# Optimization experiments

Measured on AMD Instinct MI355X. Metric: run time of the kernel, lower is better.

## Reference

```python
import jax, jax.numpy as jnp
import numpy as np

DIM = 1536
NH = 12
HD = DIM // NH          # 128
C = HD // 2             # 64 rotary pairs
F, H, W = 6, 20, 20
L = F * H * W           # 2400
B = 1
MAX_POS = 1024
EPS = 1e-6


def _rope_freqs():
    """[MAX_POS, C, 2, 2] rotation matrices, split [22,21,21] across f/h/w axes."""
    c0 = C - 2 * (C // 3)           # 22
    c1 = C // 3                      # 21
    pos = np.arange(MAX_POS, dtype=np.float32)
    parts = []
    for m in (c0, c1, c1):
        inv = 1.0 / (10000.0 ** (np.arange(m, dtype=np.float32) / m))
        parts.append(pos[:, None] * inv[None, :])
    ang = np.concatenate(parts, axis=1)          # [MAX_POS, C]
    cos, sin = np.cos(ang), np.sin(ang)
    # R[..., j, k]: rows [cos, -sin], [sin, cos]
    R = np.stack([np.stack([cos, -sin], -1), np.stack([sin, cos], -1)], -2)
    return jnp.asarray(R, dtype=jnp.float32)


def setup_inputs() -> dict:
    key = jax.random.key(0)
    ks = jax.random.split(key, 12)
    s = 1.0 / np.sqrt(DIM)
    lin = lambda k: (jax.random.normal(k, (DIM, DIM), jnp.float32) * s)
    return {
        "x": jax.random.normal(ks[0], (B, L, DIM), jnp.float32),
        "Wq": lin(ks[1]), "bq": jax.random.normal(ks[2], (DIM,), jnp.float32) * 0.01,
        "Wk": lin(ks[3]), "bk": jax.random.normal(ks[4], (DIM,), jnp.float32) * 0.01,
        "Wv": lin(ks[5]), "bv": jax.random.normal(ks[6], (DIM,), jnp.float32) * 0.01,
        "Wo": lin(ks[7]), "bo": jax.random.normal(ks[8], (DIM,), jnp.float32) * 0.01,
        "gq": jnp.ones((DIM,), jnp.float32),
        "gk": jnp.ones((DIM,), jnp.float32),
        "seq_lens": jnp.full((B,), L, dtype=jnp.int32),
        "grid_sizes": jnp.asarray([[F, H, W]], dtype=jnp.int32),
        "freqs": _rope_freqs(),
    }


def _rms_norm(x, g, eps=EPS):
    # WanRMSNorm: x * rsqrt(mean(x^2, -1) + eps) * weight
    return x * jax.lax.rsqrt(jnp.mean(jnp.square(x), axis=-1, keepdims=True) + eps) * g


def _rope_apply(xh, grid_sizes, freqs):
    """xh: [B, L, n, d]; freqs: [MAX_POS, c, 2, 2]. All samples share one grid."""
    b, l, n, d = xh.shape
    c = d // 2
    c0 = c - 2 * (c // 3)
    c1 = c // 3
    f, h, w = (int(v) for v in np.asarray(grid_sizes[0]))
    # build per-position 3D rotation matrices: [f*h*w, c, 2, 2]
    fa = jnp.broadcast_to(freqs[:f, :c0][:, None, None], (f, h, w, c0, 2, 2))
    fb = jnp.broadcast_to(freqs[:h, c0:c0 + c1][None, :, None], (f, h, w, c1, 2, 2))
    fc = jnp.broadcast_to(freqs[:w, c0 + c1:c][None, None, :], (f, h, w, c1, 2, 2))
    R = jnp.concatenate([fa, fb, fc], axis=3).reshape(f * h * w, c, 2, 2)
    xp = xh.reshape(b, l, n, c, 2)
    out = jnp.einsum('lcjk,blnck->blncj', R, xp)
    return out.reshape(b, l, n, d)


def reference(x, Wq, bq, Wk, bk, Wv, bv, Wo, bo, gq, gk, seq_lens, grid_sizes, freqs):
    b, l = x.shape[:2]
    q = _rms_norm(x @ Wq.T + bq, gq).reshape(b, l, NH, HD)
    k = _rms_norm(x @ Wk.T + bk, gk).reshape(b, l, NH, HD)
    v = (x @ Wv.T + bv).reshape(b, l, NH, HD)
    q = _rope_apply(q, grid_sizes, freqs)
    k = _rope_apply(k, grid_sizes, freqs)
    # full attention with key-length mask (window_size=(-1,-1))
    scores = jnp.einsum('bqnd,bknd->bnqk', q, k) / np.sqrt(HD)
    kmask = jnp.arange(l)[None, :] < seq_lens[:, None]          # [B, L]
    scores = jnp.where(kmask[:, None, None, :], scores, -1e9)
    attn = jax.nn.softmax(scores, axis=-1)
    out = jnp.einsum('bnqk,bknd->bqnd', attn, v).reshape(b, l, DIM)
    return out @ Wo.T + bo
```

## Files before the change

kernel.cpp:

```cpp
#include <hip/hip_runtime.h>
#include <hip/hip_bf16.h>
#include <stdint.h>


#define DIM  1536
#define NH   12
#define HD   128
#define LSEQ 2400
#define LPAD 2432
#define KT   64
#define NT   (LPAD / KT)

typedef __attribute__((ext_vector_type(8))) short short8;
typedef __attribute__((ext_vector_type(4))) float f32x4;
typedef unsigned short ushort_t;
typedef unsigned int   uint32;

__device__ __forceinline__ ushort_t f2bf(float f) {
  union { float f; unsigned u; } v; v.f = f;
  unsigned r = (v.u + 0x7fffu + ((v.u >> 16) & 1u)) >> 16;
  return (ushort_t)r;
}
__device__ __forceinline__ float bf2f(ushort_t h) {
  union { unsigned u; float f; } v; v.u = ((unsigned)h) << 16;
  return v.f;
}
__device__ __forceinline__ void async16(void* lds, const void* g) {
  __builtin_amdgcn_global_load_lds(
      (const __attribute__((address_space(1))) uint32*)g,
      (__attribute__((address_space(3))) uint32*)lds, 16, 0, 0);
}

__global__ void cvtx(const float* __restrict__ s, ushort_t* __restrict__ d)
{
  const int i = blockIdx.x * 256 + threadIdx.x;
  uint4 u = {0, 0, 0, 0};
  if (i * 8 < LSEQ * DIM) {
    float4 f0 = *(const float4*)(s + i * 8);
    float4 f1 = *(const float4*)(s + i * 8 + 4);
    u.x = (uint32)f2bf(f0.x) | ((uint32)f2bf(f0.y) << 16);
    u.y = (uint32)f2bf(f0.z) | ((uint32)f2bf(f0.w) << 16);
    u.z = (uint32)f2bf(f1.x) | ((uint32)f2bf(f1.y) << 16);
    u.w = (uint32)f2bf(f1.z) | ((uint32)f2bf(f1.w) << 16);
  }
  *(uint4*)(d + i * 8) = u;
}

__global__ void cvtw(const float* __restrict__ s0, const float* __restrict__ s1,
                     const float* __restrict__ s2, const float* __restrict__ s3,
                     ushort_t* __restrict__ d0, ushort_t* __restrict__ d1,
                     ushort_t* __restrict__ d2, ushort_t* __restrict__ d3)
{
  const int z = blockIdx.y;
  const float* s = (z == 0) ? s0 : ((z == 1) ? s1 : ((z == 2) ? s2 : s3));
  ushort_t* d    = (z == 0) ? d0 : ((z == 1) ? d1 : ((z == 2) ? d2 : d3));
  const int i = blockIdx.x * 256 + threadIdx.x;
  float4 f0 = *(const float4*)(s + i * 8);
  float4 f1 = *(const float4*)(s + i * 8 + 4);
  uint4 u;
  u.x = (uint32)f2bf(f0.x) | ((uint32)f2bf(f0.y) << 16);
  u.y = (uint32)f2bf(f0.z) | ((uint32)f2bf(f0.w) << 16);
  u.z = (uint32)f2bf(f1.x) | ((uint32)f2bf(f1.y) << 16);
  u.w = (uint32)f2bf(f1.z) | ((uint32)f2bf(f1.w) << 16);
  *(uint4*)(d + i * 8) = u;
}

template<int OUT_F32>
__global__ __launch_bounds__(256) void gemm_bt(
    const ushort_t* __restrict__ Ap,
    const ushort_t* __restrict__ B0, const ushort_t* __restrict__ B1, const ushort_t* __restrict__ B2,
    const float* __restrict__ b0, const float* __restrict__ b1, const float* __restrict__ b2,
    void* __restrict__ D0, void* __restrict__ D1, void* __restrict__ D2,
    int Mout)
{
  const int z = blockIdx.y;
  const ushort_t* Bw  = (z == 0) ? B0 : ((z == 1) ? B1 : B2);
  const float* bias   = (z == 0) ? b0 : ((z == 1) ? b1 : b2);
  void* D             = (z == 0) ? D0 : ((z == 1) ? D1 : D2);

  const int bm = blockIdx.x / 12, bn = blockIdx.x % 12;
  const int tid = threadIdx.x;
  const int w = tid >> 6, lam = tid & 63;
  const int wr = w >> 1, wc = w & 1;
  const int lane15 = lam & 15, quad = lam >> 4;

  __shared__ __align__(16) char lds[32768];
  char* sA = lds;
  char* sB = lds + 16384;

  f32x4 acc[4][4];
#pragma unroll
  for (int i = 0; i < 4; ++i)
#pragma unroll
    for (int j = 0; j < 4; ++j) acc[i][j] = {};

  const int sm = (w * 32) + (lam >> 3);
  const int sc = (lam & 7);

  for (int k0 = 0; k0 < DIM; k0 += 64) {
    __syncthreads();
#pragma unroll
    for (int i = 0; i < 4; ++i) {
      const int li = w * 4096 + i * 1024;
      const int m = sm + i * 8;
      const int c = sc ^ (m & 7);
      async16(sA + li, Ap + (size_t)(bm * 128 + m) * DIM + k0 + c * 8);
      async16(sB + li, Bw + (size_t)(bn * 128 + m) * DIM + k0 + c * 8);
    }
    __syncthreads();
#pragma unroll
    for (int kc = 0; kc < 2; ++kc) {
      const int chunk = kc * 4 + quad;
      short8 af[4], bfr[4];
#pragma unroll
      for (int i = 0; i < 4; ++i) {
        const int m = wr * 64 + i * 16 + lane15;
        af[i] = *(const short8*)(sA + m * 128 + ((chunk ^ (m & 7)) * 16));
      }
#pragma unroll
      for (int j = 0; j < 4; ++j) {
        const int n = wc * 64 + j * 16 + lane15;
        bfr[j] = *(const short8*)(sB + n * 128 + ((chunk ^ (n & 7)) * 16));
      }
#pragma unroll
      for (int i = 0; i < 4; ++i)
#pragma unroll
        for (int j = 0; j < 4; ++j)
          acc[i][j] = __builtin_amdgcn_mfma_f32_16x16x32_bf16(af[i], bfr[j], acc[i][j], 0, 0, 0);
    }
  }

#pragma unroll
  for (int j = 0; j < 4; ++j) {
    const int n = bn * 128 + wc * 64 + j * 16 + lane15;
    const float bv = bias[n];
#pragma unroll
    for (int i = 0; i < 4; ++i) {
      const int mb = bm * 128 + wr * 64 + i * 16 + quad * 4;
#pragma unroll
      for (int r = 0; r < 4; ++r) {
        const int m = mb + r;
        const float val = acc[i][j][r] + bv;
        if (OUT_F32) {
          if (m < Mout) ((float*)D)[(size_t)m * DIM + n] = val;
        } else {
          ((ushort_t*)D)[(size_t)m * DIM + n] = f2bf(val);
        }
      }
    }
  }
}

__global__ __launch_bounds__(256) void norm_rope(
    const ushort_t* __restrict__ qpre, const ushort_t* __restrict__ kpre,
    const float* __restrict__ gq, const float* __restrict__ gk,
    const float* __restrict__ freqs,
    const int* __restrict__ seq_lens, const int* __restrict__ grid_sizes,
    ushort_t* __restrict__ qh, ushort_t* __restrict__ kh)
{
  const int row = blockIdx.x;
  const int which = blockIdx.y;
  const ushort_t* src = which ? kpre : qpre;
  const float* g = which ? gk : gq;
  ushort_t* dst = which ? kh : qh;
  const int tid = threadIdx.x;

  float s = 0.f;
  if (tid < 192) {
    uint4 u = *(const uint4*)(src + (size_t)row * DIM + tid * 8);
    const uint32 uu[4] = {u.x, u.y, u.z, u.w};
#pragma unroll
    for (int i = 0; i < 4; ++i) {
      float a = bf2f((ushort_t)(uu[i] & 0xffff));
      float b = bf2f((ushort_t)(uu[i] >> 16));
      s += a * a + b * b;
    }
  }
#pragma unroll
  for (int off = 32; off; off >>= 1) s += __shfl_down(s, off, 64);
  __shared__ float wsum[4];
  __shared__ float srstd;
  if ((tid & 63) == 0) wsum[tid >> 6] = s;
  __syncthreads();
  if (tid == 0)
    srstd = rsqrtf((wsum[0] + wsum[1] + wsum[2] + wsum[3]) / (float)DIM + 1e-6f);
  __syncthreads();
  const float rstd = srstd;

  const int seq = seq_lens[0];
  const int h_ = grid_sizes[1], w_ = grid_sizes[2];
  const int hw = h_ * w_;
  const int fidx = row / hw;
  const int rem = row - fidx * hw;
  const int hidx = rem / w_;
  const int widx = rem - hidx * w_;
  const bool live = row < seq;

#pragma unroll
  for (int pp = 0; pp < 3; ++pp) {
    const int p = tid + pp * 256;
    const int c = p & 63, head = p >> 6;
    const int e_in = head * HD + 2 * c;
    uint32 xin = *(const uint32*)(src + (size_t)row * DIM + e_in);
    float x0 = bf2f((ushort_t)(xin & 0xffff));
    float x1 = bf2f((ushort_t)(xin >> 16));
    float2 gg = *(const float2*)(g + e_in);
    float y0 = x0 * rstd * gg.x, y1 = x1 * rstd * gg.y;
    const int pos = (c < 22) ? fidx : ((c < 43) ? hidx : widx);
    float4 R = *(const float4*)(freqs + ((size_t)pos * 64 + c) * 4);
    float o0 = R.x * y0 + R.y * y1;
    float o1 = R.z * y0 + R.w * y1;
    uint32 op = live ? ((uint32)f2bf(o0) | ((uint32)f2bf(o1) << 16)) : 0u;
    *(uint32*)(dst + ((size_t)head * LPAD + row) * HD + 2 * c) = op;
  }
}

__global__ void vpanel(const ushort_t* __restrict__ v, ushort_t* __restrict__ vp)
{
  const int head = blockIdx.z;
  const int d0 = blockIdx.y * 32;
  const int l0 = blockIdx.x * 32;
  __shared__ ushort_t t[32][33];
  const int tx = threadIdx.x, ty = threadIdx.y;
  t[ty][tx] = v[(size_t)(l0 + ty) * DIM + head * HD + d0 + tx];
  __syncthreads();
  const int tt = l0 >> 6;
  const int kk = (l0 & 63) + tx;
  vp[(((size_t)head * NT + tt) * HD + d0 + ty) * KT + kk] = t[tx][ty];
}

__global__ __launch_bounds__(256, 2) void attn4(
    const ushort_t* __restrict__ qh, const ushort_t* __restrict__ kh,
    const ushort_t* __restrict__ vp, const int* __restrict__ seq_lens,
    ushort_t* __restrict__ attno)
{
  const int head = blockIdx.y;
  const int q0 = blockIdx.x * 64;
  const int tid = threadIdx.x;
  const int w = tid >> 6, lam = tid & 63;
  const int lane15 = lam & 15, quad = lam >> 4;
  const int seq = seq_lens[0];

  __shared__ __align__(16) char kbuf[2][16384];
  __shared__ __align__(16) char vbuf[2][16384];
  __shared__ __align__(16) ushort_t pbuf[4][16][72];

  const ushort_t* qbase = qh + ((size_t)head * LPAD + q0 + w * 16) * HD;
  short8 qf[4];
#pragma unroll
  for (int kc = 0; kc < 4; ++kc)
    qf[kc] = *(const short8*)(qbase + lane15 * HD + kc * 32 + quad * 8);

  f32x4 o[8];
#pragma unroll
  for (int dt = 0; dt < 8; ++dt) o[dt] = {};
  float lacc[4] = {0.f, 0.f, 0.f, 0.f};

  const float scale = 0.08838834764831845f;

  const ushort_t* khh = kh + (size_t)head * LPAD * HD;
  const ushort_t* vph = vp + (size_t)head * NT * HD * KT;

  const int krow0 = w * 16 + (lam >> 4);
  const int kslot = lam & 15;
  const int vrow0 = w * 32 + (lam >> 3);
  const int vslot = lam & 7;

#define STAGE(t, b)                                                      \
  {                                                                      \
    const ushort_t* kg = khh + (size_t)(t) * (KT * HD);                  \
    const ushort_t* vg = vph + (size_t)(t) * (HD * KT);                  \
    _Pragma("unroll")                                                    \
    for (int i = 0; i < 4; ++i) {                                        \
      const int li = w * 4096 + i * 1024;                                \
      const int kr = krow0 + i * 4;                                      \
      const int kc_ = kslot ^ (kr & 15);                                 \
      async16(kbuf[b] + li, kg + kr * HD + kc_ * 8);                     \
      const int vr = vrow0 + i * 8;                                      \
      const int vc = vslot ^ (vr & 7);                                   \
      async16(vbuf[b] + li, vg + vr * KT + vc * 8);                      \
    }                                                                    \
  }

  STAGE(0, 0)
  __syncthreads();

  for (int t = 0; t < NT; ++t) {
    const int b = t & 1;
    if (t + 1 < NT) STAGE(t + 1, b ^ 1)

    f32x4 S[4];
#pragma unroll
    for (int n0 = 0; n0 < 4; ++n0) S[n0] = {};
#pragma unroll
    for (int n0 = 0; n0 < 4; ++n0)
#pragma unroll
      for (int kc = 0; kc < 4; ++kc) {
        short8 kf = *(const short8*)(kbuf[b] + (n0 * 16 + lane15) * 256 +
                                     (((kc * 4 + quad) ^ lane15) * 16));
        S[n0] = __builtin_amdgcn_mfma_f32_16x16x32_bf16(qf[kc], kf, S[n0], 0, 0, 0);
      }

#pragma unroll
    for (int n0 = 0; n0 < 4; ++n0) {
      const bool valid = (t * KT + n0 * 16 + lane15) < seq;
#pragma unroll
      for (int r = 0; r < 4; ++r) {
        float e = valid ? __expf(S[n0][r] * scale - 12.0f) : 0.f;
        lacc[r] += e;
        pbuf[w][quad * 4 + r][n0 * 16 + lane15] = f2bf(e);
      }
    }
    asm volatile("s_waitcnt lgkmcnt(0)" ::: "memory");

#pragma unroll
    for (int kc2 = 0; kc2 < 2; ++kc2) {
      short8 pf = *(const short8*)(&pbuf[w][lane15][kc2 * 32 + quad * 8]);
#pragma unroll
      for (int dt = 0; dt < 8; ++dt) {
        short8 vf = *(const short8*)(vbuf[b] + (dt * 16 + lane15) * 128 +
                                     (((kc2 * 4 + quad) ^ (lane15 & 7)) * 16));
        o[dt] = __builtin_amdgcn_mfma_f32_16x16x32_bf16(pf, vf, o[dt], 0, 0, 0);
      }
    }
    __syncthreads();
  }
#undef STAGE

  float linv[4];
#pragma unroll
  for (int r = 0; r < 4; ++r) {
    float l = lacc[r];
#pragma unroll
    for (int off = 1; off < 16; off <<= 1) l += __shfl_xor(l, off, 16);
    linv[r] = 1.0f / l;
  }
#pragma unroll
  for (int dt = 0; dt < 8; ++dt)
#pragma unroll
    for (int r = 0; r < 4; ++r) {
      const int m = q0 + w * 16 + quad * 4 + r;
      attno[(size_t)m * DIM + head * HD + dt * 16 + lane15] = f2bf(o[dt][r] * linv[r]);
    }
}

extern "C" void kernel_launch(void* const* d_in, const int* in_sizes, int n_in,
                              void* d_out, int out_size, void* d_ws, size_t ws_size,
                              hipStream_t stream)
{
  const float* x  = (const float*)d_in[0];
  const float* Wq = (const float*)d_in[1];
  const float* bq = (const float*)d_in[2];
  const float* Wk = (const float*)d_in[3];
  const float* bk = (const float*)d_in[4];
  const float* Wv = (const float*)d_in[5];
  const float* bv = (const float*)d_in[6];
  const float* Wo = (const float*)d_in[7];
  const float* bo = (const float*)d_in[8];
  const float* gq = (const float*)d_in[9];
  const float* gk = (const float*)d_in[10];
  const int* seq_lens   = (const int*)d_in[11];
  const int* grid_sizes = (const int*)d_in[12];
  const float* freqs    = (const float*)d_in[13];
  float* out = (float*)d_out;

  const size_t BUF = (size_t)LPAD * DIM * 2;
  const size_t WB  = (size_t)DIM * DIM * 2;
  char* ws = (char*)d_ws;
  dim3 blk(256);

  ushort_t* xbf  = (ushort_t*)(ws);
  ushort_t* wqb  = (ushort_t*)(ws + BUF);
  ushort_t* wkb  = (ushort_t*)(ws + BUF + WB);
  ushort_t* wvb  = (ushort_t*)(ws + BUF + 2 * WB);
  ushort_t* wob  = (ushort_t*)(ws + BUF + 3 * WB);
  ushort_t* qpre = (ushort_t*)(ws + BUF + 4 * WB);
  ushort_t* kpre = (ushort_t*)(ws + 2 * BUF + 4 * WB);
  ushort_t* qh   = (ushort_t*)(ws + 3 * BUF + 4 * WB);
  ushort_t* kh   = (ushort_t*)(ws + 4 * BUF + 4 * WB);
  ushort_t* vbf  = (ushort_t*)(ws + 5 * BUF + 4 * WB);
  ushort_t* vp    = kpre;
  ushort_t* attno = xbf;

  cvtx<<<dim3(LPAD * DIM / 2048), blk, 0, stream>>>(x, xbf);
  cvtw<<<dim3(DIM * DIM / 2048, 4), blk, 0, stream>>>(
      Wq, Wk, Wv, Wo, wqb, wkb, wvb, wob);

  gemm_bt<0><<<dim3(228, 3), blk, 0, stream>>>(
      xbf, wqb, wkb, wvb, bq, bk, bv, qpre, kpre, vbf, 0);
  norm_rope<<<dim3(LPAD, 2), blk, 0, stream>>>(
      qpre, kpre, gq, gk, freqs, seq_lens, grid_sizes, qh, kh);
  vpanel<<<dim3(LPAD / 32, HD / 32, NH), dim3(32, 32), 0, stream>>>(vbf, vp);
  attn4<<<dim3(LPAD / 64, NH), blk, 0, stream>>>(qh, kh, vp, seq_lens, attno);
  gemm_bt<1><<<dim3(228, 1), blk, 0, stream>>>(
      attno, wob, wob, wob, bo, bo, bo, out, out, out, LSEQ);
}
```

Baseline: 303.3 us.

## Split attention over two key halves with merge kernel; fuse conversion and prep kernels

Attention now splits the key sequence into two halves along a new grid dimension, doubling the block count from 456 to 912 so the GPU's compute units stay busier. Each half writes fp16 partial outputs plus row sums, and a new merge kernel combines them into bf16. The key tile shrinks to 32 and the V panel layout changes to match. The x and weight conversions are fused into one launch, and norm/rope is fused with the V transpose, cutting launches. This adds extra global traffic for the fp16 partials and the merge pass, plus some fp16 precision loss.

```diff
diff --git a/kernel.cpp b/kernel.cpp
--- a/kernel.cpp
+++ b/kernel.cpp
@@ -8,10 +8,13 @@
 #define HD   128
 #define LSEQ 2400
 #define LPAD 2432
-#define KT   64
-#define NT   (LPAD / KT)
+#define KT2  32
+#define NT2  (LPAD / KT2)
+#define NTH  38
+#define KVH  (LPAD / 2)
 
 typedef __attribute__((ext_vector_type(8))) short short8;
+typedef __attribute__((ext_vector_type(8))) _Float16 half8;
 typedef __attribute__((ext_vector_type(4))) float f32x4;
 typedef unsigned short ushort_t;
 typedef unsigned int   uint32;
@@ -30,39 +33,42 @@
       (const __attribute__((address_space(1))) uint32*)g,
       (__attribute__((address_space(3))) uint32*)lds, 16, 0, 0);
 }
-
-__global__ void cvtx(const float* __restrict__ s, ushort_t* __restrict__ d)
-{
+__device__ __forceinline__ uint4 pack8(const float* f) {
+  uint4 u;
+  u.x = (uint32)f2bf(f[0]) | ((uint32)f2bf(f[1]) << 16);
+  u.y = (uint32)f2bf(f[2]) | ((uint32)f2bf(f[3]) << 16);
+  u.z = (uint32)f2bf(f[4]) | ((uint32)f2bf(f[5]) << 16);
+  u.w = (uint32)f2bf(f[6]) | ((uint32)f2bf(f[7]) << 16);
+  return u;
+}
+
+__global__ void cvt_all(const float* __restrict__ x,
+                        const float* __restrict__ W0, const float* __restrict__ W1,
+                        const float* __restrict__ W2, const float* __restrict__ W3,
+                        ushort_t* __restrict__ xd,
+                        ushort_t* __restrict__ d0, ushort_t* __restrict__ d1,
+                        ushort_t* __restrict__ d2, ushort_t* __restrict__ d3)
+{
+  const int z = blockIdx.y;
   const int i = blockIdx.x * 256 + threadIdx.x;
-  uint4 u = {0, 0, 0, 0};
-  if (i * 8 < LSEQ * DIM) {
-    float4 f0 = *(const float4*)(s + i * 8);
-    float4 f1 = *(const float4*)(s + i * 8 + 4);
-    u.x = (uint32)f2bf(f0.x) | ((uint32)f2bf(f0.y) << 16);
-    u.y = (uint32)f2bf(f0.z) | ((uint32)f2bf(f0.w) << 16);
-    u.z = (uint32)f2bf(f1.x) | ((uint32)f2bf(f1.y) << 16);
-    u.w = (uint32)f2bf(f1.z) | ((uint32)f2bf(f1.w) << 16);
-  }
-  *(uint4*)(d + i * 8) = u;
-}
-
-__global__ void cvtw(const float* __restrict__ s0, const float* __restrict__ s1,
-                     const float* __restrict__ s2, const float* __restrict__ s3,
-                     ushort_t* __restrict__ d0, ushort_t* __restrict__ d1,
-                     ushort_t* __restrict__ d2, ushort_t* __restrict__ d3)
-{
-  const int z = blockIdx.y;
-  const float* s = (z == 0) ? s0 : ((z == 1) ? s1 : ((z == 2) ? s2 : s3));
-  ushort_t* d    = (z == 0) ? d0 : ((z == 1) ? d1 : ((z == 2) ? d2 : d3));
-  const int i = blockIdx.x * 256 + threadIdx.x;
-  float4 f0 = *(const float4*)(s + i * 8);
-  float4 f1 = *(const float4*)(s + i * 8 + 4);
-  uint4 u;
-  u.x = (uint32)f2bf(f0.x) | ((uint32)f2bf(f0.y) << 16);
-  u.y = (uint32)f2bf(f0.z) | ((uint32)f2bf(f0.w) << 16);
-  u.z = (uint32)f2bf(f1.x) | ((uint32)f2bf(f1.y) << 16);
-  u.w = (uint32)f2bf(f1.z) | ((uint32)f2bf(f1.w) << 16);
-  *(uint4*)(d + i * 8) = u;
+  if (z == 0) {
+    uint4 u = {0, 0, 0, 0};
+    if (i * 8 < LSEQ * DIM) {
+      float f[8];
+      *(float4*)f = *(const float4*)(x + i * 8);
+      *(float4*)(f + 4) = *(const float4*)(x + i * 8 + 4);
+      u = pack8(f);
+    }
+    *(uint4*)(xd + i * 8) = u;
+    return;
+  }
+  if (blockIdx.x >= DIM * DIM / 2048) return;
+  const float* s = (z == 1) ? W0 : ((z == 2) ? W1 : ((z == 3) ? W2 : W3));
+  ushort_t* d    = (z == 1) ? d0 : ((z == 2) ? d1 : ((z == 3) ? d2 : d3));
+  float f[8];
+  *(float4*)f = *(const float4*)(s + i * 8);
+  *(float4*)(f + 4) = *(const float4*)(s + i * 8 + 4);
+  *(uint4*)(d + i * 8) = pack8(f);
 }
 
 template<int OUT_F32>
@@ -151,19 +157,46 @@
   }
 }
 
-__global__ __launch_bounds__(256) void norm_rope(
+__global__ __launch_bounds__(256) void nr_vp(
     const ushort_t* __restrict__ qpre, const ushort_t* __restrict__ kpre,
+    const ushort_t* __restrict__ vbf,
     const float* __restrict__ gq, const float* __restrict__ gk,
     const float* __restrict__ freqs,
     const int* __restrict__ seq_lens, const int* __restrict__ grid_sizes,
-    ushort_t* __restrict__ qh, ushort_t* __restrict__ kh)
-{
-  const int row = blockIdx.x;
-  const int which = blockIdx.y;
+    ushort_t* __restrict__ qh, ushort_t* __restrict__ kh,
+    ushort_t* __restrict__ vp)
+{
+  const int bx = blockIdx.x;
+  const int tid = threadIdx.x;
+  __shared__ float wsum[4];
+  __shared__ float srstd;
+  __shared__ ushort_t tbuf[32][33];
+
+  if (bx >= 2 * LPAD) {
+    const int vb = bx - 2 * LPAD;
+    const int head = vb / (NT2 * 4);
+    const int rem = vb - head * (NT2 * 4);
+    const int t2 = rem >> 2;
+    const int d0 = (rem & 3) * 32;
+    const int l0 = t2 * 32;
+    const int tx = tid & 31, ty = tid >> 5;
+#pragma unroll
+    for (int rr = 0; rr < 4; ++rr)
+      tbuf[ty * 4 + rr][tx] = vbf[(size_t)(l0 + ty * 4 + rr) * DIM + head * HD + d0 + tx];
+    __syncthreads();
+#pragma unroll
+    for (int rr = 0; rr < 4; ++rr) {
+      const int d = d0 + ty * 4 + rr;
+      vp[(((size_t)head * NT2 + t2) * HD + d) * KT2 + tx] = tbuf[tx][ty * 4 + rr];
+    }
+    return;
+  }
+
+  const int row = bx >> 1;
+  const int which = bx & 1;
   const ushort_t* src = which ? kpre : qpre;
   const float* g = which ? gk : gq;
   ushort_t* dst = which ? kh : qh;
-  const int tid = threadIdx.x;
 
   float s = 0.f;
   if (tid < 192) {
@@ -178,8 +211,6 @@
   }
 #pragma unroll
   for (int off = 32; off; off >>= 1) s += __shfl_down(s, off, 64);
-  __shared__ float wsum[4];
-  __shared__ float srstd;
   if ((tid & 63) == 0) wsum[tid >> 6] = s;
   __syncthreads();
   if (tid == 0)
@@ -215,35 +246,24 @@
   }
 }
 
-__global__ void vpanel(const ushort_t* __restrict__ v, ushort_t* __restrict__ vp)
-{
-  const int head = blockIdx.z;
-  const int d0 = blockIdx.y * 32;
-  const int l0 = blockIdx.x * 32;
-  __shared__ ushort_t t[32][33];
-  const int tx = threadIdx.x, ty = threadIdx.y;
-  t[ty][tx] = v[(size_t)(l0 + ty) * DIM + head * HD + d0 + tx];
-  __syncthreads();
-  const int tt = l0 >> 6;
-  const int kk = (l0 & 63) + tx;
-  vp[(((size_t)head * NT + tt) * HD + d0 + ty) * KT + kk] = t[tx][ty];
-}
-
-__global__ __launch_bounds__(256, 2) void attn4(
+__global__ __launch_bounds__(256, 2) void attn6(
     const ushort_t* __restrict__ qh, const ushort_t* __restrict__ kh,
     const ushort_t* __restrict__ vp, const int* __restrict__ seq_lens,
-    ushort_t* __restrict__ attno)
-{
+    _Float16* __restrict__ opA, _Float16* __restrict__ opB,
+    float* __restrict__ lp)
+{
+  const int half = blockIdx.z;
   const int head = blockIdx.y;
   const int q0 = blockIdx.x * 64;
   const int tid = threadIdx.x;
   const int w = tid >> 6, lam = tid & 63;
   const int lane15 = lam & 15, quad = lam >> 4;
   const int seq = seq_lens[0];
-
-  __shared__ __align__(16) char kbuf[2][16384];
-  __shared__ __align__(16) char vbuf[2][16384];
-  __shared__ __align__(16) ushort_t pbuf[4][16][72];
+  _Float16* op = half ? opB : opA;
+
+  __shared__ __align__(16) char kbuf[2][8192];
+  __shared__ __align__(16) char vbuf[2][8192];
+  __shared__ __align__(16) ushort_t pbuf[4][16][40];
 
   const ushort_t* qbase = qh + ((size_t)head * LPAD + q0 + w * 16) * HD;
   short8 qf[4];
@@ -259,41 +279,41 @@
   const float scale = 0.08838834764831845f;
 
   const ushort_t* khh = kh + (size_t)head * LPAD * HD;
-  const ushort_t* vph = vp + (size_t)head * NT * HD * KT;
-
-  const int krow0 = w * 16 + (lam >> 4);
+  const ushort_t* vph = vp + (size_t)head * NT2 * HD * KT2;
+
+  const int krow0 = w * 8 + (lam >> 4);
   const int kslot = lam & 15;
-  const int vrow0 = w * 32 + (lam >> 3);
-  const int vslot = lam & 7;
-
-#define STAGE(t, b)                                                      \
+  const int vrow0 = w * 32 + (lam >> 2);
+  const int vslot = lam & 3;
+
+#define STAGE(gt, b)                                                     \
   {                                                                      \
-    const ushort_t* kg = khh + (size_t)(t) * (KT * HD);                  \
-    const ushort_t* vg = vph + (size_t)(t) * (HD * KT);                  \
+    const ushort_t* kg = khh + (size_t)(gt) * (KT2 * HD);                \
+    const ushort_t* vg = vph + (size_t)(gt) * (HD * KT2);                \
     _Pragma("unroll")                                                    \
-    for (int i = 0; i < 4; ++i) {                                        \
-      const int li = w * 4096 + i * 1024;                                \
+    for (int i = 0; i < 2; ++i) {                                        \
+      const int li = w * 2048 + i * 1024;                                \
       const int kr = krow0 + i * 4;                                      \
       const int kc_ = kslot ^ (kr & 15);                                 \
       async16(kbuf[b] + li, kg + kr * HD + kc_ * 8);                     \
-      const int vr = vrow0 + i * 8;                                      \
-      const int vc = vslot ^ (vr & 7);                                   \
-      async16(vbuf[b] + li, vg + vr * KT + vc * 8);                      \
+      const int vr = vrow0 + i * 16;                                     \
+      const int vc = vslot ^ (vr & 3);                                   \
+      async16(vbuf[b] + li, vg + vr * KT2 + vc * 8);                     \
     }                                                                    \
   }
 
-  STAGE(0, 0)
+  STAGE(half * NTH, 0)
   __syncthreads();
 
-  for (int t = 0; t < NT; ++t) {
+  for (int t = 0; t < NTH; ++t) {
     const int b = t & 1;
-    if (t + 1 < NT) STAGE(t + 1, b ^ 1)
-
-    f32x4 S[4];
-#pragma unroll
-    for (int n0 = 0; n0 < 4; ++n0) S[n0] = {};
-#pragma unroll
-    for (int n0 = 0; n0 < 4; ++n0)
+    const int gt = half * NTH + t;
+    if (t + 1 < NTH) STAGE(gt + 1, b ^ 1)
+
+    f32x4 S[2];
+    S[0] = {}; S[1] = {};
+#pragma unroll
+    for (int n0 = 0; n0 < 2; ++n0)
 #pragma unroll
       for (int kc = 0; kc < 4; ++kc) {
         short8 kf = *(const short8*)(kbuf[b] + (n0 * 16 + lane15) * 256 +
@@ -302,8 +322,8 @@
       }
 
 #pragma unroll
-    for (int n0 = 0; n0 < 4; ++n0) {
-      const bool valid = (t * KT + n0 * 16 + lane15) < seq;
+    for (int n0 = 0; n0 < 2; ++n0) {
+      const bool valid = (gt * KT2 + n0 * 16 + lane15) < seq;
 #pragma unroll
       for (int r = 0; r < 4; ++r) {
         float e = valid ? __expf(S[n0][r] * scale - 12.0f) : 0.f;
@@ -313,35 +333,58 @@
     }
     asm volatile("s_waitcnt lgkmcnt(0)" ::: "memory");
 
-#pragma unroll
-    for (int kc2 = 0; kc2 < 2; ++kc2) {
-      short8 pf = *(const short8*)(&pbuf[w][lane15][kc2 * 32 + quad * 8]);
-#pragma unroll
-      for (int dt = 0; dt < 8; ++dt) {
-        short8 vf = *(const short8*)(vbuf[b] + (dt * 16 + lane15) * 128 +
-                                     (((kc2 * 4 + quad) ^ (lane15 & 7)) * 16));
-        o[dt] = __builtin_amdgcn_mfma_f32_16x16x32_bf16(pf, vf, o[dt], 0, 0, 0);
-      }
+    short8 pf = *(const short8*)(&pbuf[w][lane15][quad * 8]);
+#pragma unroll
+    for (int dt = 0; dt < 8; ++dt) {
+      short8 vf = *(const short8*)(vbuf[b] + (dt * 16 + lane15) * 64 +
+                                   ((quad ^ (lane15 & 3)) * 16));
+      o[dt] = __builtin_amdgcn_mfma_f32_16x16x32_bf16(pf, vf, o[dt], 0, 0, 0);
     }
     __syncthreads();
   }
 #undef STAGE
 
-  float linv[4];
+  float lrow[4], linv[4];
 #pragma unroll
   for (int r = 0; r < 4; ++r) {
     float l = lacc[r];
 #pragma unroll
     for (int off = 1; off < 16; off <<= 1) l += __shfl_xor(l, off, 16);
+    lrow[r] = l;
     linv[r] = 1.0f / l;
+  }
+  if (lane15 == 0) {
+#pragma unroll
+    for (int r = 0; r < 4; ++r)
+      lp[((size_t)half * NH + head) * LPAD + q0 + w * 16 + quad * 4 + r] = lrow[r];
   }
 #pragma unroll
   for (int dt = 0; dt < 8; ++dt)
 #pragma unroll
     for (int r = 0; r < 4; ++r) {
       const int m = q0 + w * 16 + quad * 4 + r;
-      attno[(size_t)m * DIM + head * HD + dt * 16 + lane15] = f2bf(o[dt][r] * linv[r]);
-    }
+      op[(size_t)m * DIM + head * HD + dt * 16 + lane15] =
+          (_Float16)(o[dt][r] * linv[r]);
+    }
+}
+
+__global__ void merge(const _Float16* __restrict__ oA, const _Float16* __restrict__ oB,
+                      const float* __restrict__ lp, ushort_t* __restrict__ attno)
+{
+  const int i = blockIdx.x * 256 + threadIdx.x;
+  const int e = i * 8;
+  const int m = e / DIM;
+  const int head = (e - m * DIM) >> 7;
+  const float lA = lp[(size_t)head * LPAD + m];
+  const float lB = lp[((size_t)NH + head) * LPAD + m];
+  const float inv = 1.0f / (lA + lB);
+  const float wA = lA * inv, wB = lB * inv;
+  half8 a = *(const half8*)(oA + e);
+  half8 b = *(const half8*)(oB + e);
+  float f[8];
+#pragma unroll
+  for (int j = 0; j < 8; ++j) f[j] = (float)a[j] * wA + (float)b[j] * wB;
+  *(uint4*)(attno + e) = pack8(f);
 }
 
 extern "C" void kernel_launch(void* const* d_in, const int* in_sizes, int n_in,
@@ -379,19 +422,21 @@
   ushort_t* qh   = (ushort_t*)(ws + 3 * BUF + 4 * WB);
   ushort_t* kh   = (ushort_t*)(ws + 4 * BUF + 4 * WB);
   ushort_t* vbf  = (ushort_t*)(ws + 5 * BUF + 4 * WB);
-  ushort_t* vp    = kpre;
+  ushort_t* vp    = xbf;
   ushort_t* attno = xbf;
-
-  cvtx<<<dim3(LPAD * DIM / 2048), blk, 0, stream>>>(x, xbf);
-  cvtw<<<dim3(DIM * DIM / 2048, 4), blk, 0, stream>>>(
-      Wq, Wk, Wv, Wo, wqb, wkb, wvb, wob);
-
+  _Float16* opA = (_Float16*)qpre;
+  _Float16* opB = (_Float16*)vbf;
+  float*    lp  = (float*)wvb;
+
+  cvt_all<<<dim3(LPAD * DIM / 2048, 5), blk, 0, stream>>>(
+      x, Wq, Wk, Wv, Wo, xbf, wqb, wkb, wvb, wob);
   gemm_bt<0><<<dim3(228, 3), blk, 0, stream>>>(
       xbf, wqb, wkb, wvb, bq, bk, bv, qpre, kpre, vbf, 0);
-  norm_rope<<<dim3(LPAD, 2), blk, 0, stream>>>(
-      qpre, kpre, gq, gk, freqs, seq_lens, grid_sizes, qh, kh);
-  vpanel<<<dim3(LPAD / 32, HD / 32, NH), dim3(32, 32), 0, stream>>>(vbf, vp);
-  attn4<<<dim3(LPAD / 64, NH), blk, 0, stream>>>(qh, kh, vp, seq_lens, attno);
+  nr_vp<<<dim3(2 * LPAD + NH * NT2 * 4), blk, 0, stream>>>(
+      qpre, kpre, vbf, gq, gk, freqs, seq_lens, grid_sizes, qh, kh, vp);
+  attn6<<<dim3(LPAD / 64, NH, 2), blk, 0, stream>>>(
+      qh, kh, vp, seq_lens, opA, opB, lp);
+  merge<<<dim3(LPAD * DIM / 2048), blk, 0, stream>>>(opA, opB, lp, attno);
   gemm_bt<1><<<dim3(228, 1), blk, 0, stream>>>(
       attno, wob, wob, wob, bo, bo, bo, out, out, out, LSEQ);
 }
```

After: 296.9 us. -2.1%, faster.
